# Kernel tuning notes

Hardware: AMD Instinct MI355X
Metric: run time of the kernel (lower is better)

Reference implementation:

```python
import jax, jax.numpy as jnp
import numpy as np

N = 100000      # nodes
E = 1600000     # edges (avg degree 16)
ND = 64         # node feature dim (fiber degree-0 channels)
ED = 32         # edge feature dim
L = 3           # number of edge_update layers (num_layers - 1)
IN = ED + 2 * ND  # concat dim = 160
EPS = 1e-5
NEG_SLOPE = 0.01  # torch LeakyReLU default


def setup_inputs() -> dict:
    key = jax.random.key(0)
    ks = jax.random.split(key, 6)
    node_feat = jax.random.normal(ks[0], (N, ND), jnp.float32)
    edge_w = jax.random.normal(ks[1], (E, ED), jnp.float32)
    edge_i = jax.random.randint(ks[2], (E,), 0, N, jnp.int32)
    edge_j = jax.random.randint(ks[3], (E,), 0, N, jnp.int32)
    ln_g = jnp.ones((L, IN), jnp.float32)
    ln_b = jnp.zeros((L, IN), jnp.float32)
    w1 = jax.random.normal(ks[4], (L, IN, ED), jnp.float32) / np.sqrt(IN).astype(np.float32)
    b1 = jnp.zeros((L, ED), jnp.float32)
    w2 = jax.random.normal(ks[5], (L, ED, ED), jnp.float32) / np.sqrt(ED).astype(np.float32)
    b2 = jnp.zeros((L, ED), jnp.float32)
    return {"node_feat": node_feat, "edge_w": edge_w, "ln_g": ln_g, "ln_b": ln_b,
            "w1": w1, "b1": b1, "w2": w2, "b2": b2,
            "edge_i": edge_i, "edge_j": edge_j}


def _edge_update(nf, e, g, b, W1, B1, W2, B2, i, j):
    # gather per-edge endpoint features, concat with edge feature: [E, IN]
    x = jnp.concatenate([nf[i], nf[j], e], axis=-1)
    # LayerNorm over last dim
    mu = jnp.mean(x, axis=-1, keepdims=True)
    var = jnp.var(x, axis=-1, keepdims=True)
    x = (x - mu) * jax.lax.rsqrt(var + EPS) * g + b
    # Linear -> LeakyReLU -> Linear
    x = x @ W1 + B1
    x = jnp.where(x > 0, x, NEG_SLOPE * x)
    x = x @ W2 + B2
    return e + x  # residual edge update


def reference(node_feat, edge_w, ln_g, ln_b, w1, b1, w2, b2, edge_i, edge_j):
    e = edge_w
    for l in range(ln_g.shape[0]):  # small fixed layer count
        e = _edge_update(node_feat, e, ln_g[l], ln_b[l], w1[l], b1[l], w2[l], b2[l], edge_i, edge_j)
    return e
```

## Files before the change

### kernel.cpp

```cpp
#include <hip/hip_runtime.h>

#define EE     1600000
#define NN     100000
#define NDIM   64
#define EDIM   32
#define NLAYER 3
#define INDIM  160
#define TPB    256

static_assert(EE % TPB == 0, "grid must divide evenly");

__global__ __launch_bounds__(TPB) void node_precompute(
  const float* __restrict__ nf,  const float* __restrict__ lng,
  const float* __restrict__ lnb, const float* __restrict__ w1,
  const float* __restrict__ b1,
  float* __restrict__ P, float* __restrict__ nstat, float* __restrict__ cvec)
{
  __shared__ float sW[64*EDIM];
  __shared__ float sG[64];
  const int tid  = threadIdx.x;
  const int lp   = blockIdx.y;
  const int l    = lp >> 1, part = lp & 1;

  #pragma unroll
  for (int it = 0; it < 2; ++it){
    const int c = tid + it*TPB;
    const int d = c >> 3, ks = (c & 7) * 4;
    float4 v = *(const float4*)(w1 + (size_t)l*INDIM*EDIM + (size_t)(part*64 + d)*EDIM + ks);
    float* dst = &sW[d*EDIM + ks];
    dst[0]=v.x; dst[1]=v.y; dst[2]=v.z; dst[3]=v.w;
  }
  if (tid < 16){
    float4 v = *(const float4*)(lng + l*INDIM + part*64 + tid*4);
    sG[4*tid+0]=v.x; sG[4*tid+1]=v.y; sG[4*tid+2]=v.z; sG[4*tid+3]=v.w;
  }
  __syncthreads();

  if (lp == 0 && blockIdx.x == 0 && tid < 96){
    const int ll = tid >> 5, k = tid & 31;
    const float* wl = w1 + (size_t)ll*INDIM*EDIM;
    float c2 = 0.f, c1 = b1[ll*EDIM + k];
    for (int d = 0; d < INDIM; ++d){
      const float w = wl[d*EDIM + k];
      c2 = fmaf(lng[ll*INDIM + d], w, c2);
      c1 = fmaf(lnb[ll*INDIM + d], w, c1);
    }
    cvec[ll*EDIM + k]      = c2;
    cvec[96 + ll*EDIM + k] = c1;
  }

  const int n = blockIdx.x*TPB + tid;
  if (n >= NN) return;
  const float4* px = (const float4*)(nf + (size_t)n * NDIM);

  if (lp == 0){
    float s = 0.f, q = 0.f;
    #pragma unroll 1
    for (int c = 0; c < 16; ++c){
      float4 v = px[c];
      s += v.x + v.y + v.z + v.w;
      q = fmaf(v.x,v.x,q); q = fmaf(v.y,v.y,q);
      q = fmaf(v.z,v.z,q); q = fmaf(v.w,v.w,q);
    }
    nstat[2*n] = s; nstat[2*n+1] = q;
  }

  float acc[EDIM];
  #pragma unroll
  for (int k = 0; k < EDIM; ++k) acc[k] = 0.f;
  #pragma unroll 1
  for (int c = 0; c < 16; ++c){
    float4 xv = px[c];
    const float xs[4] = {xv.x, xv.y, xv.z, xv.w};
    const int d0 = 4*c;
    #pragma unroll
    for (int u = 0; u < 4; ++u){
      const float xd = xs[u] * sG[d0 + u];
      const float4* row = (const float4*)&sW[(size_t)(d0+u)*EDIM];
      #pragma unroll
      for (int q8 = 0; q8 < 8; ++q8){
        float4 w = row[q8];
        acc[4*q8+0] = fmaf(xd, w.x, acc[4*q8+0]);
        acc[4*q8+1] = fmaf(xd, w.y, acc[4*q8+1]);
        acc[4*q8+2] = fmaf(xd, w.z, acc[4*q8+2]);
        acc[4*q8+3] = fmaf(xd, w.w, acc[4*q8+3]);
      }
    }
  }
  float* dst = P + ((size_t)l*NN + n)*64 + part*EDIM;
  #pragma unroll
  for (int q8 = 0; q8 < 8; ++q8)
    ((float4*)dst)[q8] = make_float4(acc[4*q8+0], acc[4*q8+1], acc[4*q8+2], acc[4*q8+3]);
}

__global__ __launch_bounds__(TPB, 4) void edge_mlp_pre(
  const float* __restrict__ ew, const float* __restrict__ lng,
  const float* __restrict__ w1, const float* __restrict__ w2,
  const float* __restrict__ b2,
  const int* __restrict__ ei, const int* __restrict__ ej,
  const float* __restrict__ P, const float* __restrict__ nstat,
  const float* __restrict__ cvec, float* __restrict__ out)
{
  __shared__ float sW1E[NLAYER*EDIM*EDIM];
  __shared__ float sW2 [NLAYER*EDIM*EDIM];
  __shared__ float sGE [NLAYER*EDIM];
  __shared__ float sC2 [NLAYER*EDIM], sC1b[NLAYER*EDIM], sB2v[NLAYER*EDIM];

  const int tid = threadIdx.x;
  #pragma unroll
  for (int it = 0; it < 3; ++it){
    const int c = tid + it*TPB;
    const int l = c >> 8, rem = c & 255;
    const int d = rem >> 3, ks = (rem & 7) * 4;
    float4 v = *(const float4*)(w1 + (size_t)l*INDIM*EDIM + (size_t)(128+d)*EDIM + ks);
    float* dst = &sW1E[l*EDIM*EDIM + d*EDIM + ks];
    dst[0]=v.x; dst[1]=v.y; dst[2]=v.z; dst[3]=v.w;
  }
  #pragma unroll
  for (int it = 0; it < 3; ++it){
    const int c = tid + it*TPB;
    float4 v = ((const float4*)w2)[c];
    float* dst = &sW2[4*c];
    dst[0]=v.x; dst[1]=v.y; dst[2]=v.z; dst[3]=v.w;
  }
  if (tid < 96){
    sGE [tid] = lng[(tid>>5)*INDIM + 128 + (tid&31)];
    sB2v[tid] = b2[tid];
    sC2 [tid] = cvec[tid];
    sC1b[tid] = cvec[96 + tid];
  }
  __syncthreads();

  const int id = blockIdx.x * TPB + tid;
  const int i = ei[id], j = ej[id];

  const float2 sti = *(const float2*)(nstat + 2*(size_t)i);
  const float2 stj = *(const float2*)(nstat + 2*(size_t)j);
  const float sn = sti.x + stj.x, qn = sti.y + stj.y;

  float e[EDIM];
  {
    const float4* a = (const float4*)(ew + (size_t)id * EDIM);
    #pragma unroll
    for (int c = 0; c < 8; ++c){
      float4 v = a[c];
      e[4*c+0]=v.x; e[4*c+1]=v.y; e[4*c+2]=v.z; e[4*c+3]=v.w;
    }
  }

  #pragma unroll 1
  for (int l = 0; l < NLAYER; ++l){
    const float* Pl = P + (size_t)l * NN * 64;
    const float4* av = (const float4*)(Pl + (size_t)i*64);
    const float4* bv = (const float4*)(Pl + (size_t)j*64 + EDIM);

    float S[EDIM];
    #pragma unroll
    for (int c = 0; c < 8; ++c){
      float4 u = av[c], v = bv[c];
      S[4*c+0]=u.x+v.x; S[4*c+1]=u.y+v.y; S[4*c+2]=u.z+v.z; S[4*c+3]=u.w+v.w;
    }

    float se = 0.f, qe = 0.f;
    #pragma unroll
    for (int d = 0; d < EDIM; ++d){
      se += e[d]; qe = fmaf(e[d], e[d], qe);
    }
    const float mu = (sn + se) * (1.f/INDIM);
    const float va = fmaxf(fmaf(-mu, mu, (qn + qe) * (1.f/INDIM)), 0.f);
    const float rs = rsqrtf(va + 1e-5f);
    const float nm = -mu * rs;

    const float* wE = &sW1E[l*EDIM*EDIM];
    const float* gE = &sGE[l*EDIM];
    #pragma unroll
    for (int d = 0; d < EDIM; ++d){
      const float xd = gE[d]*e[d];
      const float4* row = (const float4*)&wE[d*EDIM];
      #pragma unroll
      for (int q = 0; q < 8; ++q){
        float4 w = row[q];
        S[4*q+0]=fmaf(xd,w.x,S[4*q+0]);
        S[4*q+1]=fmaf(xd,w.y,S[4*q+1]);
        S[4*q+2]=fmaf(xd,w.z,S[4*q+2]);
        S[4*q+3]=fmaf(xd,w.w,S[4*q+3]);
      }
    }

    const float* c2  = &sC2 [l*EDIM];
    const float* c1b = &sC1b[l*EDIM];
    const float* bb2 = &sB2v[l*EDIM];
    #pragma unroll
    for (int k = 0; k < EDIM; ++k){
      float a = fmaf(rs, S[k], fmaf(nm, c2[k], c1b[k]));
      S[k] = fmaxf(a, 0.01f*a);
    }
    #pragma unroll
    for (int k = 0; k < EDIM; ++k) e[k] += bb2[k];

    const float* w2l = &sW2[l*EDIM*EDIM];
    #pragma unroll
    for (int d = 0; d < EDIM; ++d){
      const float a = S[d];
      const float4* row = (const float4*)&w2l[d*EDIM];
      #pragma unroll
      for (int q = 0; q < 8; ++q){
        float4 w = row[q];
        e[4*q+0]=fmaf(a,w.x,e[4*q+0]);
        e[4*q+1]=fmaf(a,w.y,e[4*q+1]);
        e[4*q+2]=fmaf(a,w.z,e[4*q+2]);
        e[4*q+3]=fmaf(a,w.w,e[4*q+3]);
      }
    }
  }

  float4* o = (float4*)(out + (size_t)id * EDIM);
  #pragma unroll
  for (int c = 0; c < 8; ++c)
    o[c] = make_float4(e[4*c+0], e[4*c+1], e[4*c+2], e[4*c+3]);
}

#define EPT    2
#define EPB    (TPB*EPT)
static_assert(EE % EPB == 0, "grid must divide evenly");

__global__ __launch_bounds__(TPB, 2) void edge_mlp_fused(
  const float* __restrict__ nf,  const float* __restrict__ ew,
  const float* __restrict__ lng, const float* __restrict__ lnb,
  const float* __restrict__ w1,  const float* __restrict__ b1,
  const float* __restrict__ w2,  const float* __restrict__ b2,
  const int* __restrict__ ei, const int* __restrict__ ej,
  float* __restrict__ out)
{
  __shared__ float sW1[INDIM*EDIM];
  __shared__ float sW2[EDIM*EDIM];
  __shared__ float sC2[EDIM], sC1b[EDIM], sB2[EDIM];

  const int tid = threadIdx.x;
  const int id0 = blockIdx.x * EPB + tid;
  const int id1 = id0 + TPB;

  const float4* pi0 = (const float4*)(nf + (size_t)ei[id0] * NDIM);
  const float4* pj0 = (const float4*)(nf + (size_t)ej[id0] * NDIM);
  const float4* pi1 = (const float4*)(nf + (size_t)ei[id1] * NDIM);
  const float4* pj1 = (const float4*)(nf + (size_t)ej[id1] * NDIM);

  float e0[EDIM], e1[EDIM];
  {
    const float4* a = (const float4*)(ew + (size_t)id0 * EDIM);
    const float4* b = (const float4*)(ew + (size_t)id1 * EDIM);
    #pragma unroll
    for (int c = 0; c < 8; ++c){
      float4 v = a[c];
      e0[4*c+0]=v.x; e0[4*c+1]=v.y; e0[4*c+2]=v.z; e0[4*c+3]=v.w;
      float4 u = b[c];
      e1[4*c+0]=u.x; e1[4*c+1]=u.y; e1[4*c+2]=u.z; e1[4*c+3]=u.w;
    }
  }

  #pragma unroll 1
  for (int l = 0; l < NLAYER; ++l){
    __syncthreads();
    const float* w1l = w1 + (size_t)l * INDIM * EDIM;

    #pragma unroll
    for (int it = 0; it < 5; ++it){
      const int c = tid + it * TPB;
      const int d = c >> 3, ks = (c & 7) * 4;
      float4 v = *(const float4*)(w1l + d * EDIM + ks);
      const float g = lng[l * INDIM + d];
      sW1[d*EDIM+ks+0] = g*v.x; sW1[d*EDIM+ks+1] = g*v.y;
      sW1[d*EDIM+ks+2] = g*v.z; sW1[d*EDIM+ks+3] = g*v.w;
    }
    {
      const int d = tid >> 3, ks = (tid & 7) * 4;
      float4 v = *(const float4*)(w2 + (size_t)l*EDIM*EDIM + d*EDIM + ks);
      sW2[d*EDIM+ks+0] = v.x; sW2[d*EDIM+ks+1] = v.y;
      sW2[d*EDIM+ks+2] = v.z; sW2[d*EDIM+ks+3] = v.w;
    }
    if (tid < EDIM){
      float c1 = b1[l*EDIM + tid];
      for (int d = 0; d < INDIM; ++d)
        c1 = fmaf(lnb[l*INDIM + d], w1l[d*EDIM + tid], c1);
      sC1b[tid] = c1;
      sB2[tid]  = b2[l*EDIM + tid];
    }
    __syncthreads();
    if (tid < EDIM){
      float s = 0.f;
      for (int d = 0; d < INDIM; ++d) s += sW1[d*EDIM + tid];
      sC2[tid] = s;
    }
    __syncthreads();

    float S0[EDIM], S1[EDIM];
    #pragma unroll
    for (int k = 0; k < EDIM; ++k){ S0[k] = 0.f; S1[k] = 0.f; }
    float sum0 = 0.f, sq0 = 0.f, sum1 = 0.f, sq1 = 0.f;

    auto dot_row = [&](float xv0, float xv1, const float4* row){
      sum0 += xv0; sq0 = fmaf(xv0, xv0, sq0);
      sum1 += xv1; sq1 = fmaf(xv1, xv1, sq1);
      #pragma unroll
      for (int q = 0; q < 8; ++q){
        float4 w = row[q];
        S0[4*q+0] = fmaf(xv0, w.x, S0[4*q+0]); S1[4*q+0] = fmaf(xv1, w.x, S1[4*q+0]);
        S0[4*q+1] = fmaf(xv0, w.y, S0[4*q+1]); S1[4*q+1] = fmaf(xv1, w.y, S1[4*q+1]);
        S0[4*q+2] = fmaf(xv0, w.z, S0[4*q+2]); S1[4*q+2] = fmaf(xv1, w.z, S1[4*q+2]);
        S0[4*q+3] = fmaf(xv0, w.w, S0[4*q+3]); S1[4*q+3] = fmaf(xv1, w.w, S1[4*q+3]);
      }
    };

    #pragma unroll 1
    for (int c = 0; c < 32; ++c){
      const float4 x0 = (c < 16) ? pi0[c] : pj0[c - 16];
      const float4 x1 = (c < 16) ? pi1[c] : pj1[c - 16];
      const float4* wr = (const float4*)&sW1[c * 4 * EDIM];
      dot_row(x0.x, x1.x, wr + 0);
      dot_row(x0.y, x1.y, wr + 8);
      dot_row(x0.z, x1.z, wr + 16);
      dot_row(x0.w, x1.w, wr + 24);
    }
    #pragma unroll
    for (int d = 0; d < EDIM; ++d){
      const float4* row = (const float4*)&sW1[(2*NDIM + d) * EDIM];
      dot_row(e0[d], e1[d], row);
    }

    const float mu0 = sum0 * (1.f/INDIM);
    const float va0 = fmaxf(fmaf(-mu0, mu0, sq0 * (1.f/INDIM)), 0.f);
    const float rs0 = rsqrtf(va0 + 1e-5f);
    const float nm0 = -mu0 * rs0;
    const float mu1 = sum1 * (1.f/INDIM);
    const float va1 = fmaxf(fmaf(-mu1, mu1, sq1 * (1.f/INDIM)), 0.f);
    const float rs1 = rsqrtf(va1 + 1e-5f);
    const float nm1 = -mu1 * rs1;

    float h0[EDIM], h1v[EDIM];
    #pragma unroll
    for (int k = 0; k < EDIM; ++k){
      float a = fmaf(rs0, S0[k], fmaf(nm0, sC2[k], sC1b[k]));
      h0[k]  = fmaxf(a, 0.01f * a);
      float b = fmaf(rs1, S1[k], fmaf(nm1, sC2[k], sC1b[k]));
      h1v[k] = fmaxf(b, 0.01f * b);
    }
    #pragma unroll
    for (int k = 0; k < EDIM; ++k){ e0[k] += sB2[k]; e1[k] += sB2[k]; }
    #pragma unroll
    for (int d = 0; d < EDIM; ++d){
      const float a = h0[d], b = h1v[d];
      const float4* row = (const float4*)&sW2[d * EDIM];
      #pragma unroll
      for (int q = 0; q < 8; ++q){
        float4 w = row[q];
        e0[4*q+0] = fmaf(a, w.x, e0[4*q+0]); e1[4*q+0] = fmaf(b, w.x, e1[4*q+0]);
        e0[4*q+1] = fmaf(a, w.y, e0[4*q+1]); e1[4*q+1] = fmaf(b, w.y, e1[4*q+1]);
        e0[4*q+2] = fmaf(a, w.z, e0[4*q+2]); e1[4*q+2] = fmaf(b, w.z, e1[4*q+2]);
        e0[4*q+3] = fmaf(a, w.w, e0[4*q+3]); e1[4*q+3] = fmaf(b, w.w, e1[4*q+3]);
      }
    }
  }

  float4* o0 = (float4*)(out + (size_t)id0 * EDIM);
  float4* o1 = (float4*)(out + (size_t)id1 * EDIM);
  #pragma unroll
  for (int c = 0; c < 8; ++c){
    o0[c] = make_float4(e0[4*c+0], e0[4*c+1], e0[4*c+2], e0[4*c+3]);
    o1[c] = make_float4(e1[4*c+0], e1[4*c+1], e1[4*c+2], e1[4*c+3]);
  }
}

extern "C" void kernel_launch(void* const* d_in, const int* in_sizes, int n_in,
                              void* d_out, int out_size, void* d_ws, size_t ws_size,
                              hipStream_t stream)
{
  const float* nf  = (const float*)d_in[0];
  const float* ew  = (const float*)d_in[1];
  const float* lng = (const float*)d_in[2];
  const float* lnb = (const float*)d_in[3];
  const float* w1  = (const float*)d_in[4];
  const float* b1  = (const float*)d_in[5];
  const float* w2  = (const float*)d_in[6];
  const float* b2  = (const float*)d_in[7];
  const int*   ei  = (const int*)d_in[8];
  const int*   ej  = (const int*)d_in[9];
  float* out = (float*)d_out;

  const size_t PBYTES = (size_t)NLAYER * NN * 64 * sizeof(float);
  const size_t SBYTES = (size_t)NN * 2 * sizeof(float);
  const size_t CBYTES = (size_t)2 * NLAYER * EDIM * sizeof(float);

  if (d_ws && ws_size >= PBYTES + SBYTES + CBYTES){
    float* P     = (float*)d_ws;
    float* nstat = (float*)((char*)d_ws + PBYTES);
    float* cvec  = (float*)((char*)d_ws + PBYTES + SBYTES);
    hipLaunchKernelGGL(node_precompute,
                       dim3((NN + TPB - 1)/TPB, 6), dim3(TPB), 0, stream,
                       nf, lng, lnb, w1, b1, P, nstat, cvec);
    hipLaunchKernelGGL(edge_mlp_pre, dim3(EE / TPB), dim3(TPB), 0, stream,
                       ew, lng, w1, w2, b2, ei, ej, P, nstat, cvec, out);
  } else {
    dim3 grid(EE / EPB), block(TPB);
    hipLaunchKernelGGL(edge_mlp_fused, grid, block, 0, stream,
                       nf, ew, lng, lnb, w1, b1, w2, b2, ei, ej, out);
  }
}
```

Measured before the change: 898.9 us.

## Read edge MLP weights from global via scalar loads instead of LDS staging

New measurement: 1.432 ms. 1.59x slower.

```diff
diff --git a/kernel.cpp b/kernel.cpp
--- a/kernel.cpp
+++ b/kernel.cpp
@@ -14,7 +14,8 @@
   const float* __restrict__ nf,  const float* __restrict__ lng,
   const float* __restrict__ lnb, const float* __restrict__ w1,
   const float* __restrict__ b1,
-  float* __restrict__ P, float* __restrict__ nstat, float* __restrict__ cvec)
+  float* __restrict__ P, float* __restrict__ nstat, float* __restrict__ cvec,
+  float* __restrict__ wtab)
 {
   __shared__ float sW[64*EDIM];
   __shared__ float sG[64];
@@ -48,6 +49,15 @@
     cvec[ll*EDIM + k]      = c2;
     cvec[96 + ll*EDIM + k] = c1;
   }
+  if (lp == 1 && blockIdx.x == 0){
+    #pragma unroll
+    for (int it = 0; it < 12; ++it){
+      const int c = tid + it*TPB;
+      const int ll = c >> 10, rem = c & 1023;
+      const int d = rem >> 5, k = rem & 31;
+      wtab[c] = lng[ll*INDIM + 128 + d] * w1[(size_t)ll*INDIM*EDIM + (size_t)(128+d)*EDIM + k];
+    }
+  }
 
   const int n = blockIdx.x*TPB + tid;
   if (n >= NN) return;
@@ -93,44 +103,15 @@
     ((float4*)dst)[q8] = make_float4(acc[4*q8+0], acc[4*q8+1], acc[4*q8+2], acc[4*q8+3]);
 }
 
-__global__ __launch_bounds__(TPB, 4) void edge_mlp_pre(
-  const float* __restrict__ ew, const float* __restrict__ lng,
-  const float* __restrict__ w1, const float* __restrict__ w2,
-  const float* __restrict__ b2,
+__global__ __launch_bounds__(TPB, 6) void edge_mlp_pre(
+  const float* __restrict__ ew,
+  const float* __restrict__ w2, const float* __restrict__ b2,
   const int* __restrict__ ei, const int* __restrict__ ej,
   const float* __restrict__ P, const float* __restrict__ nstat,
-  const float* __restrict__ cvec, float* __restrict__ out)
+  const float* __restrict__ cvec, const float* __restrict__ wtab,
+  float* __restrict__ out)
 {
-  __shared__ float sW1E[NLAYER*EDIM*EDIM];
-  __shared__ float sW2 [NLAYER*EDIM*EDIM];
-  __shared__ float sGE [NLAYER*EDIM];
-  __shared__ float sC2 [NLAYER*EDIM], sC1b[NLAYER*EDIM], sB2v[NLAYER*EDIM];
-
   const int tid = threadIdx.x;
-  #pragma unroll
-  for (int it = 0; it < 3; ++it){
-    const int c = tid + it*TPB;
-    const int l = c >> 8, rem = c & 255;
-    const int d = rem >> 3, ks = (rem & 7) * 4;
-    float4 v = *(const float4*)(w1 + (size_t)l*INDIM*EDIM + (size_t)(128+d)*EDIM + ks);
-    float* dst = &sW1E[l*EDIM*EDIM + d*EDIM + ks];
-    dst[0]=v.x; dst[1]=v.y; dst[2]=v.z; dst[3]=v.w;
-  }
-  #pragma unroll
-  for (int it = 0; it < 3; ++it){
-    const int c = tid + it*TPB;
-    float4 v = ((const float4*)w2)[c];
-    float* dst = &sW2[4*c];
-    dst[0]=v.x; dst[1]=v.y; dst[2]=v.z; dst[3]=v.w;
-  }
-  if (tid < 96){
-    sGE [tid] = lng[(tid>>5)*INDIM + 128 + (tid&31)];
-    sB2v[tid] = b2[tid];
-    sC2 [tid] = cvec[tid];
-    sC1b[tid] = cvec[96 + tid];
-  }
-  __syncthreads();
-
   const int id = blockIdx.x * TPB + tid;
   const int i = ei[id], j = ej[id];
 
@@ -171,12 +152,11 @@
     const float rs = rsqrtf(va + 1e-5f);
     const float nm = -mu * rs;
 
-    const float* wE = &sW1E[l*EDIM*EDIM];
-    const float* gE = &sGE[l*EDIM];
-    #pragma unroll
-    for (int d = 0; d < EDIM; ++d){
-      const float xd = gE[d]*e[d];
-      const float4* row = (const float4*)&wE[d*EDIM];
+    const float* wE = wtab + l*EDIM*EDIM;
+    #pragma unroll
+    for (int d = 0; d < EDIM; ++d){
+      const float xd = e[d];
+      const float4* row = (const float4*)(wE + d*EDIM);
       #pragma unroll
       for (int q = 0; q < 8; ++q){
         float4 w = row[q];
@@ -187,9 +167,9 @@
       }
     }
 
-    const float* c2  = &sC2 [l*EDIM];
-    const float* c1b = &sC1b[l*EDIM];
-    const float* bb2 = &sB2v[l*EDIM];
+    const float* c2  = cvec + l*EDIM;
+    const float* c1b = cvec + 96 + l*EDIM;
+    const float* bb2 = b2 + l*EDIM;
     #pragma unroll
     for (int k = 0; k < EDIM; ++k){
       float a = fmaf(rs, S[k], fmaf(nm, c2[k], c1b[k]));
@@ -198,11 +178,11 @@
     #pragma unroll
     for (int k = 0; k < EDIM; ++k) e[k] += bb2[k];
 
-    const float* w2l = &sW2[l*EDIM*EDIM];
+    const float* w2l = w2 + (size_t)l*EDIM*EDIM;
     #pragma unroll
     for (int d = 0; d < EDIM; ++d){
       const float a = S[d];
-      const float4* row = (const float4*)&w2l[d*EDIM];
+      const float4* row = (const float4*)(w2l + d*EDIM);
       #pragma unroll
       for (int q = 0; q < 8; ++q){
         float4 w = row[q];
@@ -389,16 +369,18 @@
   const size_t PBYTES = (size_t)NLAYER * NN * 64 * sizeof(float);
   const size_t SBYTES = (size_t)NN * 2 * sizeof(float);
   const size_t CBYTES = (size_t)2 * NLAYER * EDIM * sizeof(float);
-
-  if (d_ws && ws_size >= PBYTES + SBYTES + CBYTES){
+  const size_t WBYTES = (size_t)NLAYER * EDIM * EDIM * sizeof(float);
+
+  if (d_ws && ws_size >= PBYTES + SBYTES + CBYTES + WBYTES){
     float* P     = (float*)d_ws;
     float* nstat = (float*)((char*)d_ws + PBYTES);
     float* cvec  = (float*)((char*)d_ws + PBYTES + SBYTES);
+    float* wtab  = (float*)((char*)d_ws + PBYTES + SBYTES + CBYTES);
     hipLaunchKernelGGL(node_precompute,
                        dim3((NN + TPB - 1)/TPB, 6), dim3(TPB), 0, stream,
-                       nf, lng, lnb, w1, b1, P, nstat, cvec);
+                       nf, lng, lnb, w1, b1, P, nstat, cvec, wtab);
     hipLaunchKernelGGL(edge_mlp_pre, dim3(EE / TPB), dim3(TPB), 0, stream,
-                       ew, lng, w1, w2, b2, ei, ej, P, nstat, cvec, out);
+                       ew, w2, b2, ei, ej, P, nstat, cvec, wtab, out);
   } else {
     dim3 grid(EE / EPB), block(TPB);
     hipLaunchKernelGGL(edge_mlp_fused, grid, block, 0, stream,
```
